# Performance work log

Hardware: AMD Instinct MI355X
Metric: run time of the kernel (lower is better)

Reference implementation:

```python
import jax, jax.numpy as jnp
import numpy as np

K = 8            # NEAREST_K
IN = 68          # input_size = 64 + 4
EO = 32          # edge_output_size
FEAT = IN * 2 + EO * 4  # 264
EMB = 32         # linear_embedding
NCLS = 2
N = 768
EPS = 1e-5


def lrelu(x):
    return jnp.where(x >= 0, x, 0.01 * x)


def setup_inputs() -> dict:
    key = jax.random.key(0)
    ks = jax.random.split(key, 16)

    def w(k, fan_in, fan_out):
        return jax.random.normal(k, (fan_in, fan_out), jnp.float32) / np.float32(np.sqrt(fan_in))

    return {
        "feat0": jax.random.normal(ks[0], (N, IN), jnp.float32),
        "feat1": jax.random.normal(ks[1], (N, IN), jnp.float32),
        # edge_conv1: Linear(IN*K, EO) -> LeakyReLU -> Linear(EO, EO) -> LeakyReLU
        "ec1_w1": w(ks[2], IN * K, EO), "ec1_b1": jnp.zeros((EO,), jnp.float32),
        "ec1_w2": w(ks[3], EO, EO),     "ec1_b2": jnp.zeros((EO,), jnp.float32),
        # edge_conv2: Linear(EO*K, EO) -> LeakyReLU -> Linear(EO, EO) -> LeakyReLU
        "ec2_w1": w(ks[4], EO * K, EO), "ec2_b1": jnp.zeros((EO,), jnp.float32),
        "ec2_w2": w(ks[5], EO, EO),     "ec2_b2": jnp.zeros((EO,), jnp.float32),
        # linear head: BN(FEAT) -> Linear(FEAT,EMB) -> LReLU -> Linear(EMB,EMB) -> LReLU -> Linear(EMB,NCLS)
        "bn_g": jnp.ones((FEAT,), jnp.float32), "bn_b": jnp.zeros((FEAT,), jnp.float32),
        "lin1_w": w(ks[6], FEAT, EMB), "lin1_b": jnp.zeros((EMB,), jnp.float32),
        "lin2_w": w(ks[7], EMB, EMB),  "lin2_b": jnp.zeros((EMB,), jnp.float32),
        "lin3_w": w(ks[8], EMB, NCLS), "lin3_b": jnp.zeros((NCLS,), jnp.float32),
    }


def _pairs_for_graph(feat, ec1_w1, ec1_b1, ec1_w2, ec1_b2,
                     ec2_w1, ec2_b1, ec2_w2, ec2_b2):
    n = feat.shape[0]
    # kNN on first 4 dims via pairwise L1 distance (includes self, dist 0)
    coords = feat[:, :4]
    dist = jnp.abs(coords[:, None, :] - coords[None, :, :]).sum(-1)  # [n, n]
    _, idx = jax.lax.top_k(-dist, K)  # [n, K] smallest distances

    # EdgeConv 1: gather neighbor features, flatten feature-major (matches torch transpose+view)
    e1 = feat[idx]                                  # [n, K, IN]
    e1 = jnp.swapaxes(e1, 1, 2).reshape(n, IN * K)  # [n, IN*K]
    e1 = lrelu(lrelu(e1 @ ec1_w1 + ec1_b1) @ ec1_w2 + ec1_b2)  # [n, EO]

    # EdgeConv 2 on edge1 outputs
    e2 = e1[idx]                                    # [n, K, EO]
    e2 = jnp.swapaxes(e2, 1, 2).reshape(n, EO * K)  # [n, EO*K]
    e2 = lrelu(lrelu(e2 @ ec2_w1 + ec2_b1) @ ec2_w2 + ec2_b2)  # [n, EO]

    x = jnp.concatenate([feat, e1, e2], axis=-1)    # [n, IN + 2*EO] = [n, 132]
    # upper-triangle (i<j) all-pairs concat, row-major order == torch masked_select of triu mask
    iu, ju = jnp.triu_indices(n, k=1)
    return jnp.concatenate([x[iu], x[ju]], axis=-1)  # [n(n-1)/2, FEAT]


def reference(feat0, feat1, ec1_w1, ec1_b1, ec1_w2, ec1_b2,
              ec2_w1, ec2_b1, ec2_w2, ec2_b2,
              bn_g, bn_b, lin1_w, lin1_b, lin2_w, lin2_b, lin3_w, lin3_b):
    ec = (ec1_w1, ec1_b1, ec1_w2, ec1_b2, ec2_w1, ec2_b1, ec2_w2, ec2_b2)
    x = jnp.concatenate([_pairs_for_graph(feat0, *ec),
                         _pairs_for_graph(feat1, *ec)], axis=0)  # [P, FEAT]
    # BatchNorm1d in training mode: batch statistics (biased variance)
    mu = x.mean(axis=0)
    var = x.var(axis=0)
    x = (x - mu) * jax.lax.rsqrt(var + EPS) * bn_g + bn_b
    x = lrelu(x @ lin1_w + lin1_b)
    x = lrelu(x @ lin2_w + lin2_b)
    return x @ lin3_w + lin3_b  # [P, NCLS]
```

## Files before the change

kernel.cpp:

```cpp
#include <hip/hip_runtime.h>

#define NN 768
#define IN_F 68
#define KNN 8
#define EO 32
#define FEAT 264
#define HALF_FEAT 132
#define EMB 32
#define NPAIR 294528

typedef __attribute__((ext_vector_type(8))) short bf16x8;
typedef __attribute__((ext_vector_type(4))) float f32x4;

static __device__ __forceinline__ int pack_chop2(float x0, float x1) {
  return __builtin_amdgcn_perm(__float_as_uint(x1), __float_as_uint(x0), 0x07060302);
}
static __device__ __forceinline__ float chop(float x) {
  return __uint_as_float(__float_as_uint(x) & 0xffff0000u);
}


__global__ void __launch_bounds__(128) topk_ec1_kernel(
    const float* __restrict__ feat0, const float* __restrict__ feat1,
    const float* __restrict__ w1, const float* __restrict__ b1,
    const float* __restrict__ w2, const float* __restrict__ b2,
    int* __restrict__ idx_out, float* __restrict__ e1out)
{
  const int i = blockIdx.x, g = blockIdx.y;
  const float* __restrict__ feat = g ? feat1 : feat0;
  const int tid = threadIdx.x;
  const int lane = tid & 63, wv = tid >> 6;

  __shared__ unsigned long long keys[128*8];
  __shared__ int nbr[8];
  __shared__ float gl[KNN*IN_F];
  __shared__ float hsh[EO];
  __shared__ f32x4 part1[16][8];
  __shared__ f32x4 part2[16][8];

  const float4 ci = *(const float4*)(feat + i*IN_F);

  float4 cand[6];
#pragma unroll
  for (int t = 0; t < 6; t++)
    cand[t] = *(const float4*)(feat + (tid + 128*t)*IN_F);

  float bd[8]; int bidx[8];
#pragma unroll
  for (int k = 0; k < 8; k++) { bd[k] = 1e30f; bidx[k] = 0; }
#pragma unroll
  for (int t = 0; t < 6; t++) {
    const int j = tid + 128*t;
    float d = fabsf(ci.x - cand[t].x);
    d += fabsf(ci.y - cand[t].y);
    d += fabsf(ci.z - cand[t].z);
    d += fabsf(ci.w - cand[t].w);
    if (d < bd[7]) {
#pragma unroll
      for (int k = 7; k >= 1; k--) {
        if (d < bd[k-1])    { bd[k] = bd[k-1]; bidx[k] = bidx[k-1]; }
        else if (d < bd[k]) { bd[k] = d;       bidx[k] = j; }
      }
      if (d < bd[0]) { bd[0] = d; bidx[0] = j; }
    }
  }
#pragma unroll
  for (int k = 0; k < 8; k++)
    keys[tid*8+k] = ((unsigned long long)__float_as_uint(bd[k]) << 32) | (unsigned)bidx[k];
  __syncthreads();

  if (wv == 0) {
    int posA = 0, posB = 0;
#pragma unroll
    for (int r = 0; r < 8; r++) {
      unsigned long long ha = keys[lane*8 + posA];
      unsigned long long hb = keys[(lane+64)*8 + posB];
      unsigned long long mn = ha < hb ? ha : hb;
#pragma unroll
      for (int s = 32; s >= 1; s >>= 1) {
        unsigned long long o = __shfl_xor(mn, s, 64);
        mn = (o < mn) ? o : mn;
      }
      if (ha == mn) posA++;
      else if (hb == mn) posB++;
      if (lane == 0) {
        int nb = (int)(mn & 0xffffffffull);
        nbr[r] = nb;
        idx_out[(g*NN+i)*8 + r] = nb;
      }
    }
  }
  __syncthreads();

  for (int z = tid; z < KNN*17; z += 128) {
    int k = z / 17, q = z - k*17;
    *(float4*)&gl[k*IN_F + q*4] = *(const float4*)(feat + nbr[k]*IN_F + q*4);
  }
  __syncthreads();

  const int eg = tid & 7, sub = tid >> 3;
  {
    f32x4 a4 = {0.f,0.f,0.f,0.f};
    const float* wp = w1 + eg*4;
    for (int t = 0; t < 34; t++) {
      const int r = sub + 16*t;
      const int k = r & 7, c = r >> 3;
      const float s = gl[k*IN_F + c];
      a4 += s * *(const f32x4*)(wp + r*EO);
    }
    part1[sub][eg] = a4;
  }
  __syncthreads();
  if (tid < 32) {
    float h = b1[tid];
    const float* pp = (const float*)part1;
#pragma unroll
    for (int s = 0; s < 16; s++) h += pp[s*32 + tid];
    hsh[tid] = fmaxf(h, 0.01f*h);
  }
  __syncthreads();

  {
    const int m0 = sub*2;
    f32x4 a4 = hsh[m0]   * *(const f32x4*)(w2 + (m0+0)*EO + eg*4)
             + hsh[m0+1] * *(const f32x4*)(w2 + (m0+1)*EO + eg*4);
    part2[sub][eg] = a4;
  }
  __syncthreads();
  if (tid < 32) {
    float o = b2[tid];
    const float* pp = (const float*)part2;
#pragma unroll
    for (int s = 0; s < 16; s++) o += pp[s*32 + tid];
    o = fmaxf(o, 0.01f*o);
    e1out[(g*NN+i)*EO + tid] = o;
  }
}

__global__ void __launch_bounds__(64) ec2_kernel(
    const int* __restrict__ idx, const float* __restrict__ e1,
    const float* __restrict__ w1, const float* __restrict__ b1,
    const float* __restrict__ w2, const float* __restrict__ b2,
    float* __restrict__ e2out)
{
  const int i = blockIdx.x, g = blockIdx.y;
  const int lane = threadIdx.x;
  __shared__ float gl[KNN*36];
  __shared__ float hsh[EO];
  __shared__ f32x4 partb[8][8];
  {
    const int k = lane >> 3, q = lane & 7;
    const int nb = idx[(g*NN+i)*8 + k];
    *(float4*)&gl[k*36 + q*4] = *(const float4*)(e1 + (g*NN+nb)*EO + q*4);
  }
  __syncthreads();
  const int eg = lane & 7, sub = lane >> 3;
  {
    f32x4 a4 = {0.f,0.f,0.f,0.f};
    const float* wp = w1 + eg*4;
    for (int t = 0; t < 32; t++) {
      const int r = sub + 8*t;
      const float s = gl[sub*36 + t];
      a4 += s * *(const f32x4*)(wp + r*EO);
    }
    partb[sub][eg] = a4;
  }
  __syncthreads();
  if (lane < 32) {
    float h = b1[lane];
    const float* pp = (const float*)partb;
#pragma unroll
    for (int s = 0; s < 8; s++) h += pp[s*32 + lane];
    hsh[lane] = fmaxf(h, 0.01f*h);
  }
  __syncthreads();
  {
    f32x4 a4 = {0.f,0.f,0.f,0.f};
#pragma unroll
    for (int j = 0; j < 4; j++) {
      const int m = sub*4 + j;
      a4 += hsh[m] * *(const f32x4*)(w2 + m*EO + eg*4);
    }
    partb[sub][eg] = a4;
  }
  __syncthreads();
  if (lane < 32) {
    float o = b2[lane];
    const float* pp = (const float*)partb;
#pragma unroll
    for (int s = 0; s < 8; s++) o += pp[s*32 + lane];
    o = fmaxf(o, 0.01f*o);
    e2out[(g*NN+i)*EO + lane] = o;
  }
}

__global__ void __launch_bounds__(256) stats_kernel(
    const float* __restrict__ feat0, const float* __restrict__ feat1,
    const float* __restrict__ e1, const float* __restrict__ e2,
    const float* __restrict__ bn_g,
    float* __restrict__ mu_out, float* __restrict__ sg_out)
{
  const int c = blockIdx.x;
  const int tid = threadIdx.x;
  double s1=0, s2=0, q1=0, q2=0;
  for (int t = tid; t < 2*NN; t += 256) {
    int g = t >= NN;
    int i = t - g*NN;
    float val;
    if (c < IN_F)      val = (g ? feat1 : feat0)[i*IN_F + c];
    else if (c < 100)  val = e1[(g*NN+i)*EO + (c-IN_F)];
    else               val = e2[(g*NN+i)*EO + (c-100)];
    double dv = val;
    double wf = (double)(NN-1-i), wsnd = (double)i;
    s1 += wf*dv;  s2 += wsnd*dv;
    double dq = dv*dv;
    q1 += wf*dq;  q2 += wsnd*dq;
  }
#pragma unroll
  for (int off = 32; off >= 1; off >>= 1) {
    s1 += __shfl_xor(s1, off, 64);
    s2 += __shfl_xor(s2, off, 64);
    q1 += __shfl_xor(q1, off, 64);
    q2 += __shfl_xor(q2, off, 64);
  }
  __shared__ double red[4][4];
  const int w = tid >> 6;
  if ((tid & 63) == 0) { red[w][0]=s1; red[w][1]=s2; red[w][2]=q1; red[w][3]=q2; }
  __syncthreads();
  if (tid == 0) {
    double t0 = red[0][0]+red[1][0]+red[2][0]+red[3][0];
    double t1 = red[0][1]+red[1][1]+red[2][1]+red[3][1];
    double t2 = red[0][2]+red[1][2]+red[2][2]+red[3][2];
    double t3 = red[0][3]+red[1][3]+red[2][3]+red[3][3];
    const double M2 = 2.0 * (double)NPAIR;
    double mu1 = t0/M2, mu2 = t1/M2;
    double v1 = t2/M2 - mu1*mu1;
    double v2 = t3/M2 - mu2*mu2;
    mu_out[c]           = (float)mu1;
    mu_out[HALF_FEAT+c] = (float)mu2;
    sg_out[c]           = (float)((double)bn_g[c] / sqrt(v1 + 1e-5));
    sg_out[HALF_FEAT+c] = (float)((double)bn_g[HALF_FEAT+c] / sqrt(v2 + 1e-5));
  }
}

__global__ void __launch_bounds__(64) uv_c0_kernel(
    const float* __restrict__ feat0, const float* __restrict__ feat1,
    const float* __restrict__ e1, const float* __restrict__ e2,
    const float* __restrict__ sg, const float* __restrict__ mu,
    const float* __restrict__ bn_b,
    const float* __restrict__ lin1_w, const float* __restrict__ lin1_b,
    float* __restrict__ u, float* __restrict__ v, float* __restrict__ c0g)
{
  const int i = blockIdx.x, g = blockIdx.y;
  const int t = threadIdx.x;
  if (i == NN) {
    if (g == 0 && t < EMB) {
      float a0=0.f, a1=0.f, a2=0.f, a3=0.f;
      for (int c = 0; c < FEAT; c += 4) {
        a0 += (bn_b[c+0] - mu[c+0]*sg[c+0]) * lin1_w[(c+0)*EMB + t];
        a1 += (bn_b[c+1] - mu[c+1]*sg[c+1]) * lin1_w[(c+1)*EMB + t];
        a2 += (bn_b[c+2] - mu[c+2]*sg[c+2]) * lin1_w[(c+2)*EMB + t];
        a3 += (bn_b[c+3] - mu[c+3]*sg[c+3]) * lin1_w[(c+3)*EMB + t];
      }
      c0g[t] = lin1_b[t] + ((a0+a1)+(a2+a3));
    }
    return;
  }
  __shared__ float x[HALF_FEAT];
  __shared__ f32x4 partd[8][8];
  for (int c = t; c < IN_F; c += 64) x[c] = (g ? feat1 : feat0)[i*IN_F + c];
  if (t < 32) x[IN_F + t]     = e1[(g*NN+i)*EO + t];
  else        x[100 + (t-32)] = e2[(g*NN+i)*EO + (t-32)];
  __syncthreads();
  const int eg = t & 7, sub = t >> 3;
  {
    f32x4 a4 = {0.f,0.f,0.f,0.f};
    const int roff = (sub >= 4) ? HALF_FEAT : 0;
    const float* wp = lin1_w + eg*4;
    for (int tt = 0; tt < 33; tt++) {
      const int r = sub*33 + tt;
      const float xv = x[r - roff] * sg[r];
      a4 += xv * *(const f32x4*)(wp + r*EMB);
    }
    partd[sub][eg] = a4;
  }
  __syncthreads();
  const float* pp = (const float*)partd;
  if (t < 32) {
    float acc = (pp[0*32+t] + pp[1*32+t]) + (pp[2*32+t] + pp[3*32+t]);
    u[(g*NN+i)*EMB + t] = acc;
  } else {
    const int e = t - 32;
    float acc = (pp[4*32+e] + pp[5*32+e]) + (pp[6*32+e] + pp[7*32+e]);
    v[(g*NN+i)*EMB + e] = acc;
  }
}

__global__ void __launch_bounds__(256) pair_kernel(
    const float* __restrict__ u, const float* __restrict__ v,
    const float* __restrict__ c0g,
    const float* __restrict__ lin2_w, const float* __restrict__ lin2_b,
    const float* __restrict__ lin3_w, const float* __restrict__ lin3_b,
    float2* __restrict__ out)
{
  const int g = blockIdx.y;
  int rem = blockIdx.x;
  int a = 0;
  while (rem >= 48 - a) { rem -= 48 - a; a++; }
  const int b = a + rem;

  __shared__ float su[16*36], sv[16*36];
  __shared__ float wbuf[4][16*36];
  const int tid = threadIdx.x;
  {
    int r = tid >> 5, c = tid & 31;
    su[r*36+c] = u[(g*NN + a*16 + r)*EMB + c];
    sv[r*36+c] = v[(g*NN + b*16 + r)*EMB + c];
    r += 8;
    su[r*36+c] = u[(g*NN + a*16 + r)*EMB + c];
    sv[r*36+c] = v[(g*NN + b*16 + r)*EMB + c];
  }
  __syncthreads();

  const int lane = tid & 63, w = tid >> 6;
  const int q = lane & 15, kg = lane >> 4;

  union { int i[4]; bf16x8 v; } whi0, wlo0, whi1, wlo1;
#pragma unroll
  for (int d = 0; d < 4; d++) {
    float w0a = lin2_w[(kg*8+2*d)*32 + q];
    float w0b = lin2_w[(kg*8+2*d+1)*32 + q];
    float w1a = lin2_w[(kg*8+2*d)*32 + 16 + q];
    float w1b = lin2_w[(kg*8+2*d+1)*32 + 16 + q];
    whi0.i[d] = pack_chop2(w0a, w0b);
    wlo0.i[d] = pack_chop2(w0a - chop(w0a), w0b - chop(w0b));
    whi1.i[d] = pack_chop2(w1a, w1b);
    wlo1.i[d] = pack_chop2(w1a - chop(w1a), w1b - chop(w1b));
  }
  float svc[8];
#pragma unroll
  for (int jj = 0; jj < 8; jj++)
    svc[jj] = sv[q*36 + kg*8 + jj] + c0g[kg*8+jj];
  float2 w3v[8]; float b2v[8];
#pragma unroll
  for (int jj = 0; jj < 8; jj++) {
    w3v[jj] = ((const float2*)lin3_w)[kg*8+jj];
    b2v[jj] = lin2_b[kg*8+jj];
  }
  const float b30 = lin3_b[0], b31 = lin3_b[1];

  float* wb = wbuf[w];
#pragma unroll
  for (int t = 0; t < 4; t++) {
    const int ty = w*4 + t;
    const float4 sa = *(const float4*)&su[ty*36 + kg*8];
    const float4 sb = *(const float4*)&su[ty*36 + kg*8 + 4];
    float se[8] = {sa.x, sa.y, sa.z, sa.w, sb.x, sb.y, sb.z, sb.w};
    union { int i[4]; bf16x8 v; } ahi, alo;
#pragma unroll
    for (int d = 0; d < 4; d++) {
      float s0 = se[2*d]   + svc[2*d];
      float s1 = se[2*d+1] + svc[2*d+1];
      s0 = fmaxf(s0, 0.01f*s0);
      s1 = fmaxf(s1, 0.01f*s1);
      ahi.i[d] = pack_chop2(s0, s1);
      alo.i[d] = pack_chop2(s0 - chop(s0), s1 - chop(s1));
    }
    f32x4 acc0 = {0.f,0.f,0.f,0.f}, acc1 = {0.f,0.f,0.f,0.f};
    acc0 = __builtin_amdgcn_mfma_f32_16x16x32_bf16(ahi.v, whi0.v, acc0, 0,0,0);
    acc1 = __builtin_amdgcn_mfma_f32_16x16x32_bf16(ahi.v, whi1.v, acc1, 0,0,0);
    acc0 = __builtin_amdgcn_mfma_f32_16x16x32_bf16(ahi.v, wlo0.v, acc0, 0,0,0);
    acc1 = __builtin_amdgcn_mfma_f32_16x16x32_bf16(ahi.v, wlo1.v, acc1, 0,0,0);
    acc0 = __builtin_amdgcn_mfma_f32_16x16x32_bf16(alo.v, whi0.v, acc0, 0,0,0);
    acc1 = __builtin_amdgcn_mfma_f32_16x16x32_bf16(alo.v, whi1.v, acc1, 0,0,0);
#pragma unroll
    for (int r = 0; r < 4; r++) {
      wb[(kg*4+r)*36 + q]      = acc0[r];
      wb[(kg*4+r)*36 + 16 + q] = acc1[r];
    }
    float o0 = 0.f, o1 = 0.f;
#pragma unroll
    for (int jj = 0; jj < 8; jj++) {
      float h = wb[q*36 + kg*8 + jj] + b2v[jj];
      h = fmaxf(h, 0.01f*h);
      o0 += h * w3v[jj].x;
      o1 += h * w3v[jj].y;
    }
    o0 += __shfl_xor(o0, 16, 64); o0 += __shfl_xor(o0, 32, 64);
    o1 += __shfl_xor(o1, 16, 64); o1 += __shfl_xor(o1, 32, 64);
    const int i = a*16 + ty, j = b*16 + q;
    if (lane < 16 && j > i) {
      long p = (long)i*NN - (long)i*(i+1)/2 + (j - i - 1);
      out[(long)g*NPAIR + p] = make_float2(o0 + b30, o1 + b31);
    }
  }
}

extern "C" void kernel_launch(void* const* d_in, const int* in_sizes, int n_in,
                              void* d_out, int out_size, void* d_ws, size_t ws_size,
                              hipStream_t stream)
{
  const float* feat0  = (const float*)d_in[0];
  const float* feat1  = (const float*)d_in[1];
  const float* ec1_w1 = (const float*)d_in[2];
  const float* ec1_b1 = (const float*)d_in[3];
  const float* ec1_w2 = (const float*)d_in[4];
  const float* ec1_b2 = (const float*)d_in[5];
  const float* ec2_w1 = (const float*)d_in[6];
  const float* ec2_b1 = (const float*)d_in[7];
  const float* ec2_w2 = (const float*)d_in[8];
  const float* ec2_b2 = (const float*)d_in[9];
  const float* bn_g   = (const float*)d_in[10];
  const float* bn_b   = (const float*)d_in[11];
  const float* lin1_w = (const float*)d_in[12];
  const float* lin1_b = (const float*)d_in[13];
  const float* lin2_w = (const float*)d_in[14];
  const float* lin2_b = (const float*)d_in[15];
  const float* lin3_w = (const float*)d_in[16];
  const float* lin3_b = (const float*)d_in[17];

  char* ws = (char*)d_ws;
  int*   idx = (int*)  (ws + 0);
  float* e1  = (float*)(ws + 49152);
  float* e2  = (float*)(ws + 245760);
  float* u   = (float*)(ws + 442368);
  float* v   = (float*)(ws + 638976);
  float* mu  = (float*)(ws + 835584);
  float* sg  = (float*)(ws + 836640);
  float* c0g = (float*)(ws + 837696);

  topk_ec1_kernel<<<dim3(768,2), 128, 0, stream>>>(feat0, feat1, ec1_w1, ec1_b1,
                                                   ec1_w2, ec1_b2, idx, e1);
  ec2_kernel<<<dim3(768,2), 64, 0, stream>>>(idx, e1, ec2_w1, ec2_b1,
                                             ec2_w2, ec2_b2, e2);
  stats_kernel<<<dim3(132), 256, 0, stream>>>(feat0, feat1, e1, e2, bn_g, mu, sg);
  uv_c0_kernel<<<dim3(769,2), 64, 0, stream>>>(feat0, feat1, e1, e2, sg, mu, bn_b,
                                               lin1_w, lin1_b, u, v, c0g);
  pair_kernel<<<dim3(1176,2), 256, 0, stream>>>(u, v, c0g, lin2_w, lin2_b,
                                                lin3_w, lin3_b, (float2*)d_out);
}
```

Before: 130.7 us.

## Widen pair tiles to 16x32 and merge top-k via register bitonic shuffles

The pair kernel now computes a 16x32 tile of pairs per block instead of 16x16. This halves the block count and amortizes the per-block setup (weight packing, constant loads, shared staging) over twice as many MFMA ops. The kNN top-8 merge replaces the serial shared-memory selection done by one wave with a butterfly shuffle merge of sorted 8-lists in registers across both waves. The cost is more registers per thread and more wasted lanes on diagonal tiles.

```diff
diff --git a/kernel.cpp b/kernel.cpp
--- a/kernel.cpp
+++ b/kernel.cpp
@@ -19,6 +19,25 @@
   return __uint_as_float(__float_as_uint(x) & 0xffff0000u);
 }
 
+
+static __device__ __forceinline__ void merge8(unsigned long long k[8],
+                                              const unsigned long long o[8]) {
+  unsigned long long m[8];
+#pragma unroll
+  for (int x = 0; x < 8; x++) {
+    unsigned long long a = k[x], b = o[7-x];
+    m[x] = a < b ? a : b;
+  }
+#define CSW(p,qq) { unsigned long long lo = m[p]<m[qq]?m[p]:m[qq]; \
+                    unsigned long long hi = m[p]<m[qq]?m[qq]:m[p]; \
+                    m[p]=lo; m[qq]=hi; }
+  CSW(0,4) CSW(1,5) CSW(2,6) CSW(3,7)
+  CSW(0,2) CSW(1,3) CSW(4,6) CSW(5,7)
+  CSW(0,1) CSW(2,3) CSW(4,5) CSW(6,7)
+#undef CSW
+#pragma unroll
+  for (int x = 0; x < 8; x++) k[x] = m[x];
+}
 
 __global__ void __launch_bounds__(128) topk_ec1_kernel(
     const float* __restrict__ feat0, const float* __restrict__ feat1,
@@ -31,8 +50,8 @@
   const int tid = threadIdx.x;
   const int lane = tid & 63, wv = tid >> 6;
 
-  __shared__ unsigned long long keys[128*8];
   __shared__ int nbr[8];
+  __shared__ unsigned long long xk[2][8];
   __shared__ float gl[KNN*IN_F];
   __shared__ float hsh[EO];
   __shared__ f32x4 part1[16][8];
@@ -64,30 +83,36 @@
       if (d < bd[0]) { bd[0] = d; bidx[0] = j; }
     }
   }
+
+  unsigned long long key[8];
 #pragma unroll
   for (int k = 0; k < 8; k++)
-    keys[tid*8+k] = ((unsigned long long)__float_as_uint(bd[k]) << 32) | (unsigned)bidx[k];
-  __syncthreads();
-
-  if (wv == 0) {
-    int posA = 0, posB = 0;
-#pragma unroll
-    for (int r = 0; r < 8; r++) {
-      unsigned long long ha = keys[lane*8 + posA];
-      unsigned long long hb = keys[(lane+64)*8 + posB];
-      unsigned long long mn = ha < hb ? ha : hb;
-#pragma unroll
-      for (int s = 32; s >= 1; s >>= 1) {
-        unsigned long long o = __shfl_xor(mn, s, 64);
-        mn = (o < mn) ? o : mn;
-      }
-      if (ha == mn) posA++;
-      else if (hb == mn) posB++;
-      if (lane == 0) {
-        int nb = (int)(mn & 0xffffffffull);
-        nbr[r] = nb;
-        idx_out[(g*NN+i)*8 + r] = nb;
-      }
+    key[k] = ((unsigned long long)__float_as_uint(bd[k]) << 32) | (unsigned)bidx[k];
+
+#pragma unroll
+  for (int s = 1; s < 64; s <<= 1) {
+    unsigned long long ok[8];
+#pragma unroll
+    for (int x = 0; x < 8; x++) ok[x] = __shfl_xor(key[x], s, 64);
+    merge8(key, ok);
+  }
+  if (lane == 0) {
+#pragma unroll
+    for (int x = 0; x < 8; x++) xk[wv][x] = key[x];
+  }
+  __syncthreads();
+  {
+    unsigned long long ok[8];
+#pragma unroll
+    for (int x = 0; x < 8; x++) ok[x] = xk[wv^1][x];
+    merge8(key, ok);
+  }
+  if (tid == 0) {
+#pragma unroll
+    for (int k = 0; k < 8; k++) {
+      int nb = (int)(key[k] & 0xffffffffull);
+      nbr[k] = nb;
+      idx_out[(g*NN+i)*8 + k] = nb;
     }
   }
   __syncthreads();
@@ -305,20 +330,25 @@
 {
   const int g = blockIdx.y;
   int rem = blockIdx.x;
-  int a = 0;
-  while (rem >= 48 - a) { rem -= 48 - a; a++; }
-  const int b = a + rem;
-
-  __shared__ float su[16*36], sv[16*36];
-  __shared__ float wbuf[4][16*36];
+  int B2 = 0;
+  for (;;) {
+    int cnt = 2*B2 + 2; if (cnt > 48) cnt = 48;
+    if (rem < cnt) break;
+    rem -= cnt; B2++;
+  }
+  const int a = rem;
+
+  __shared__ float su[16*36], sv[32*36];
+  __shared__ float wbuf[4][32*36];
   const int tid = threadIdx.x;
   {
-    int r = tid >> 5, c = tid & 31;
-    su[r*36+c] = u[(g*NN + a*16 + r)*EMB + c];
-    sv[r*36+c] = v[(g*NN + b*16 + r)*EMB + c];
-    r += 8;
-    su[r*36+c] = u[(g*NN + a*16 + r)*EMB + c];
-    sv[r*36+c] = v[(g*NN + b*16 + r)*EMB + c];
+    const int r = tid >> 5, c = tid & 31;
+    su[r*36+c]      = u[(g*NN + a*16 + r)*EMB + c];
+    su[(r+8)*36+c]  = u[(g*NN + a*16 + r+8)*EMB + c];
+    sv[r*36+c]      = v[(g*NN + B2*32 + r)*EMB + c];
+    sv[(r+8)*36+c]  = v[(g*NN + B2*32 + r+8)*EMB + c];
+    sv[(r+16)*36+c] = v[(g*NN + B2*32 + r+16)*EMB + c];
+    sv[(r+24)*36+c] = v[(g*NN + B2*32 + r+24)*EMB + c];
   }
   __syncthreads();
 
@@ -337,10 +367,13 @@
     whi1.i[d] = pack_chop2(w1a, w1b);
     wlo1.i[d] = pack_chop2(w1a - chop(w1a), w1b - chop(w1b));
   }
-  float svc[8];
-#pragma unroll
-  for (int jj = 0; jj < 8; jj++)
-    svc[jj] = sv[q*36 + kg*8 + jj] + c0g[kg*8+jj];
+  float svc0[8], svc1[8];
+#pragma unroll
+  for (int jj = 0; jj < 8; jj++) {
+    const float c0 = c0g[kg*8+jj];
+    svc0[jj] = sv[q*36 + kg*8 + jj] + c0;
+    svc1[jj] = sv[(16+q)*36 + kg*8 + jj] + c0;
+  }
   float2 w3v[8]; float b2v[8];
 #pragma unroll
   for (int jj = 0; jj < 8; jj++) {
@@ -356,42 +389,70 @@
     const float4 sa = *(const float4*)&su[ty*36 + kg*8];
     const float4 sb = *(const float4*)&su[ty*36 + kg*8 + 4];
     float se[8] = {sa.x, sa.y, sa.z, sa.w, sb.x, sb.y, sb.z, sb.w};
-    union { int i[4]; bf16x8 v; } ahi, alo;
+    union { int i[4]; bf16x8 v; } ahi0, alo0, ahi1, alo1;
 #pragma unroll
     for (int d = 0; d < 4; d++) {
-      float s0 = se[2*d]   + svc[2*d];
-      float s1 = se[2*d+1] + svc[2*d+1];
+      float s0 = se[2*d]   + svc0[2*d];
+      float s1 = se[2*d+1] + svc0[2*d+1];
       s0 = fmaxf(s0, 0.01f*s0);
       s1 = fmaxf(s1, 0.01f*s1);
-      ahi.i[d] = pack_chop2(s0, s1);
-      alo.i[d] = pack_chop2(s0 - chop(s0), s1 - chop(s1));
-    }
-    f32x4 acc0 = {0.f,0.f,0.f,0.f}, acc1 = {0.f,0.f,0.f,0.f};
-    acc0 = __builtin_amdgcn_mfma_f32_16x16x32_bf16(ahi.v, whi0.v, acc0, 0,0,0);
-    acc1 = __builtin_amdgcn_mfma_f32_16x16x32_bf16(ahi.v, whi1.v, acc1, 0,0,0);
-    acc0 = __builtin_amdgcn_mfma_f32_16x16x32_bf16(ahi.v, wlo0.v, acc0, 0,0,0);
-    acc1 = __builtin_amdgcn_mfma_f32_16x16x32_bf16(ahi.v, wlo1.v, acc1, 0,0,0);
-    acc0 = __builtin_amdgcn_mfma_f32_16x16x32_bf16(alo.v, whi0.v, acc0, 0,0,0);
-    acc1 = __builtin_amdgcn_mfma_f32_16x16x32_bf16(alo.v, whi1.v, acc1, 0,0,0);
+      ahi0.i[d] = pack_chop2(s0, s1);
+      alo0.i[d] = pack_chop2(s0 - chop(s0), s1 - chop(s1));
+      float t0 = se[2*d]   + svc1[2*d];
+      float t1 = se[2*d+1] + svc1[2*d+1];
+      t0 = fmaxf(t0, 0.01f*t0);
+      t1 = fmaxf(t1, 0.01f*t1);
+      ahi1.i[d] = pack_chop2(t0, t1);
+      alo1.i[d] = pack_chop2(t0 - chop(t0), t1 - chop(t1));
+    }
+    f32x4 acc00 = {0.f,0.f,0.f,0.f}, acc01 = {0.f,0.f,0.f,0.f};
+    f32x4 acc10 = {0.f,0.f,0.f,0.f}, acc11 = {0.f,0.f,0.f,0.f};
+    acc00 = __builtin_amdgcn_mfma_f32_16x16x32_bf16(ahi0.v, whi0.v, acc00, 0,0,0);
+    acc01 = __builtin_amdgcn_mfma_f32_16x16x32_bf16(ahi0.v, whi1.v, acc01, 0,0,0);
+    acc10 = __builtin_amdgcn_mfma_f32_16x16x32_bf16(ahi1.v, whi0.v, acc10, 0,0,0);
+    acc11 = __builtin_amdgcn_mfma_f32_16x16x32_bf16(ahi1.v, whi1.v, acc11, 0,0,0);
+    acc00 = __builtin_amdgcn_mfma_f32_16x16x32_bf16(ahi0.v, wlo0.v, acc00, 0,0,0);
+    acc01 = __builtin_amdgcn_mfma_f32_16x16x32_bf16(ahi0.v, wlo1.v, acc01, 0,0,0);
+    acc10 = __builtin_amdgcn_mfma_f32_16x16x32_bf16(ahi1.v, wlo0.v, acc10, 0,0,0);
+    acc11 = __builtin_amdgcn_mfma_f32_16x16x32_bf16(ahi1.v, wlo1.v, acc11, 0,0,0);
+    acc00 = __builtin_amdgcn_mfma_f32_16x16x32_bf16(alo0.v, whi0.v, acc00, 0,0,0);
+    acc01 = __builtin_amdgcn_mfma_f32_16x16x32_bf16(alo0.v, whi1.v, acc01, 0,0,0);
+    acc10 = __builtin_amdgcn_mfma_f32_16x16x32_bf16(alo1.v, whi0.v, acc10, 0,0,0);
+    acc11 = __builtin_amdgcn_mfma_f32_16x16x32_bf16(alo1.v, whi1.v, acc11, 0,0,0);
 #pragma unroll
     for (int r = 0; r < 4; r++) {
-      wb[(kg*4+r)*36 + q]      = acc0[r];
-      wb[(kg*4+r)*36 + 16 + q] = acc1[r];
-    }
-    float o0 = 0.f, o1 = 0.f;
+      wb[(kg*4+r)*36 + q]           = acc00[r];
+      wb[(kg*4+r)*36 + 16 + q]      = acc01[r];
+      wb[(16+kg*4+r)*36 + q]        = acc10[r];
+      wb[(16+kg*4+r)*36 + 16 + q]   = acc11[r];
+    }
+    float o00 = 0.f, o01 = 0.f, o10 = 0.f, o11 = 0.f;
 #pragma unroll
     for (int jj = 0; jj < 8; jj++) {
-      float h = wb[q*36 + kg*8 + jj] + b2v[jj];
-      h = fmaxf(h, 0.01f*h);
-      o0 += h * w3v[jj].x;
-      o1 += h * w3v[jj].y;
-    }
-    o0 += __shfl_xor(o0, 16, 64); o0 += __shfl_xor(o0, 32, 64);
-    o1 += __shfl_xor(o1, 16, 64); o1 += __shfl_xor(o1, 32, 64);
-    const int i = a*16 + ty, j = b*16 + q;
-    if (lane < 16 && j > i) {
-      long p = (long)i*NN - (long)i*(i+1)/2 + (j - i - 1);
-      out[(long)g*NPAIR + p] = make_float2(o0 + b30, o1 + b31);
+      float h0 = wb[q*36 + kg*8 + jj] + b2v[jj];
+      h0 = fmaxf(h0, 0.01f*h0);
+      o00 += h0 * w3v[jj].x;
+      o01 += h0 * w3v[jj].y;
+      float h1 = wb[(16+q)*36 + kg*8 + jj] + b2v[jj];
+      h1 = fmaxf(h1, 0.01f*h1);
+      o10 += h1 * w3v[jj].x;
+      o11 += h1 * w3v[jj].y;
+    }
+    o00 += __shfl_xor(o00, 16, 64); o00 += __shfl_xor(o00, 32, 64);
+    o01 += __shfl_xor(o01, 16, 64); o01 += __shfl_xor(o01, 32, 64);
+    o10 += __shfl_xor(o10, 16, 64); o10 += __shfl_xor(o10, 32, 64);
+    o11 += __shfl_xor(o11, 16, 64); o11 += __shfl_xor(o11, 32, 64);
+    const int i = a*16 + ty;
+    if (lane < 16) {
+      const int j0 = B2*32 + q, j1 = B2*32 + 16 + q;
+      if (j0 > i) {
+        long p = (long)i*NN - (long)i*(i+1)/2 + (j0 - i - 1);
+        out[(long)g*NPAIR + p] = make_float2(o00 + b30, o01 + b31);
+      }
+      if (j1 > i) {
+        long p = (long)i*NN - (long)i*(i+1)/2 + (j1 - i - 1);
+        out[(long)g*NPAIR + p] = make_float2(o10 + b30, o11 + b31);
+      }
     }
   }
 }
@@ -436,6 +497,6 @@
   stats_kernel<<<dim3(132), 256, 0, stream>>>(feat0, feat1, e1, e2, bn_g, mu, sg);
   uv_c0_kernel<<<dim3(769,2), 64, 0, stream>>>(feat0, feat1, e1, e2, sg, mu, bn_b,
                                                lin1_w, lin1_b, u, v, c0g);
-  pair_kernel<<<dim3(1176,2), 256, 0, stream>>>(u, v, c0g, lin2_w, lin2_b,
-                                                lin3_w, lin3_b, (float2*)d_out);
-}
+  pair_kernel<<<dim3(600,2), 256, 0, stream>>>(u, v, c0g, lin2_w, lin2_b,
+                                               lin3_w, lin3_b, (float2*)d_out);
+}
```

New measurement: 130.8 us. Within noise of the previous version (+0.1%).
